# Kernel tuning notes

Measured on AMD Instinct MI355X. Metric: run time of the kernel, lower is better.

The kernel has to match this reference:

```python
import math
import jax, jax.numpy as jnp
import numpy as np

B = 1024
D = 384
Q = 65536
TOPK = 128
HARD_W = 2.0
TEMP_START = 0.2
TEMP_END = 0.05
WARMUP = 10


def _temperature(epoch):
    # curriculum cosine decay (epoch is a Python int)
    if epoch >= WARMUP:
        return TEMP_END
    progress = epoch / max(1, WARMUP)
    return TEMP_END + 0.5 * (TEMP_START - TEMP_END) * (1.0 + math.cos(math.pi * progress))


def _normalize(x):
    # F.normalize: x / max(||x||, eps)
    n = jnp.linalg.norm(x, axis=-1, keepdims=True)
    return x / jnp.maximum(n, 1e-12)


def _hard_neg_reweight(logits):
    # logits: [B, N]; labels = arange(B) (diagonal positives)
    b = logits.shape[0]
    rows = jnp.arange(b)
    neg_logits = logits.at[rows, rows].set(-jnp.inf)      # mask positives
    _, hard_idx = jax.lax.top_k(neg_logits, TOPK)          # [B, TOPK] hardest negatives
    weights = jnp.ones_like(logits)
    weights = weights.at[rows[:, None], hard_idx].set(HARD_W)
    weights = weights.at[rows, rows].set(1.0)
    return logits * weights


def _cross_entropy_diag(logits):
    b = logits.shape[0]
    logp = jax.nn.log_softmax(logits, axis=-1)
    return -jnp.mean(logp[jnp.arange(b), jnp.arange(b)])


def setup_inputs() -> dict:
    key = jax.random.key(0)
    k1, k2, k3, k4 = jax.random.split(key, 4)
    rgb_feat = jax.random.normal(k1, (B, D), dtype=jnp.float32)
    ir_feat = jax.random.normal(k2, (B, D), dtype=jnp.float32)
    rgb_queue = _normalize(jax.random.normal(k3, (Q, D), dtype=jnp.float32))
    ir_queue = _normalize(jax.random.normal(k4, (Q, D), dtype=jnp.float32))
    return {"rgb_feat": rgb_feat, "ir_feat": ir_feat,
            "rgb_queue": rgb_queue, "ir_queue": ir_queue, "epoch": 0}


def reference(rgb_feat, ir_feat, rgb_queue, ir_queue, epoch):
    temp = _temperature(epoch)
    rgb_z = _normalize(rgb_feat.astype(jnp.float32))
    ir_z = _normalize(ir_feat.astype(jnp.float32))
    ir_all = jnp.concatenate([ir_z, ir_queue], axis=0)    # [B+Q, D]
    rgb_all = jnp.concatenate([rgb_z, rgb_queue], axis=0)
    logits_r2i = (rgb_z @ ir_all.T) / temp                # [B, B+Q]
    logits_i2r = (ir_z @ rgb_all.T) / temp
    logits_r2i = _hard_neg_reweight(logits_r2i)
    logits_i2r = _hard_neg_reweight(logits_i2r)
    return 0.5 * (_cross_entropy_diag(logits_r2i) + _cross_entropy_diag(logits_i2r))
```

## Files before the change

### kernel.cpp

```cpp
#include <hip/hip_runtime.h>
#include <hip/hip_bf16.h>

#define B_    1024
#define D_    384
#define Q_    65536
#define N_    66560
#define TOPK_ 128

#define NBIN_ 4096
#define CAP_  2048

typedef __bf16 bf16x8 __attribute__((ext_vector_type(8)));
typedef float  f32x4  __attribute__((ext_vector_type(4)));
typedef unsigned short u16;
typedef u16 u16x8 __attribute__((ext_vector_type(8)));

__device__ __forceinline__ unsigned short f2bf(float x) {
  unsigned int u = __float_as_uint(x);
  unsigned int r = (u + 0x7fffu + ((u >> 16) & 1u)) >> 16;
  return (unsigned short)r;
}

__device__ __forceinline__ void gld_lds16(const void* g, void* l) {
  __builtin_amdgcn_global_load_lds(
      (__attribute__((address_space(1))) void*)(g),
      (__attribute__((address_space(3))) void*)(l), 16, 0, 0);
}

__device__ __forceinline__ void wait_vmcnt(int n) {
  switch (n) {
    case 12: asm volatile("s_waitcnt vmcnt(12)" ::: "memory"); break;
    case 6:  asm volatile("s_waitcnt vmcnt(6)"  ::: "memory"); break;
    default: asm volatile("s_waitcnt vmcnt(0)"  ::: "memory"); break;
  }
}

__device__ __forceinline__ unsigned int bf2key(unsigned int u) {
  return u ^ ((u & 0x8000u) ? 0xFFFFu : 0x8000u);
}

__global__ __launch_bounds__(64) void k_normalize(
    const float* __restrict__ rgb, const float* __restrict__ ir,
    const int* __restrict__ ep,
    u16* __restrict__ zrA, u16* __restrict__ ziA,
    u16* __restrict__ zrU, u16* __restrict__ ziU)
{
  int r = blockIdx.x & (B_ - 1);
  bool isIr = blockIdx.x >= B_;
  const float* src = (isIr ? ir : rgb) + (size_t)r * D_;
  u16* dA = (isIr ? ziA : zrA) + (size_t)r * D_;
  u16* dU = (isIr ? ziU : zrU) + (size_t)r * D_;
  int t = threadIdx.x;
  float x[6]; float ss = 0.f;
  #pragma unroll
  for (int k = 0; k < 6; ++k) { x[k] = src[t + 64*k]; ss += x[k]*x[k]; }
  #pragma unroll
  for (int off = 32; off > 0; off >>= 1) ss += __shfl_down(ss, off);
  ss = __shfl(ss, 0);
  float inv = 1.0f / fmaxf(sqrtf(ss), 1e-12f);

  int e = ep[0];
  float temp;
  if (e >= 10) temp = 0.05f;
  else {
    float p = (float)e * 0.1f;
    temp = 0.05f + 0.075f * (1.0f + cosf(3.14159265358979323846f * p));
  }
  float itemp = 1.0f / temp;

  #pragma unroll
  for (int k = 0; k < 6; ++k) {
    float z = x[k] * inv;
    dU[t + 64*k] = f2bf(z);
    dA[t + 64*k] = f2bf(z * itemp);
  }
}

__global__ __launch_bounds__(256) void k_build_ball(
    const u16* __restrict__ zU, const float* __restrict__ queue,
    u16* __restrict__ ball)
{
  size_t i = ((size_t)blockIdx.x * 256 + threadIdx.x) * 8;
  const size_t zElems = (size_t)B_ * D_;
  if (i < zElems) {
    *(uint4*)(ball + i) = *(const uint4*)(zU + i);
  } else {
    const float* q = queue + (i - zElems);
    float4 a = *(const float4*)q;
    float4 b = *(const float4*)(q + 4);
    u16x8 o;
    o[0] = f2bf(a.x); o[1] = f2bf(a.y); o[2] = f2bf(a.z); o[3] = f2bf(a.w);
    o[4] = f2bf(b.x); o[5] = f2bf(b.y); o[6] = f2bf(b.z); o[7] = f2bf(b.w);
    *(u16x8*)(ball + i) = o;
  }
}

#define BK_ 32
#define NSTEP_ 12
__global__ __launch_bounds__(256, 2) void k_gemm(
    const u16* __restrict__ A,
    const u16* __restrict__ ball,
    u16* __restrict__ C,
    float* __restrict__ diag,
    int r0, int mtiles)
{
  __shared__ __align__(16) unsigned char smem[73728];
  u16* Ct = (u16*)smem;

  int bid = blockIdx.x, nwg = gridDim.x;
  int xcd = bid & 7, loc = bid >> 3;
  int q = nwg >> 3, rr8 = nwg & 7;
  int wgid = (xcd < rr8 ? xcd * (q + 1) : rr8 * (q + 1) + (xcd - rr8) * q) + loc;
  int nt = wgid / mtiles;
  int mt = wgid - nt * mtiles;

  const int tid  = threadIdx.x;
  const int wave = tid >> 6, lane = tid & 63;
  const int mbase = mt * 128;
  const int nbase = nt * 256;
  const u16* Ab = A    + (size_t)(r0 + mbase) * D_;
  const u16* Bb = ball + (size_t)nbase * D_;

  auto As = [&](int t) -> u16* { return (u16*)(smem + (t % 3) * 24576); };
  auto Bs = [&](int t) -> u16* { return (u16*)(smem + (t % 3) * 24576 + 8192); };
  auto stage = [&](int t) {
    const int ks = t * BK_;
    #pragma unroll
    for (int i = 0; i < 2; ++i) {
      int f = i * 256 + tid;
      int rr = f >> 2, cc = f & 3;
      int koff = (((cc * 16) ^ (((rr >> 1) & 3) << 4)) >> 1);
      gld_lds16(Ab + (size_t)rr * D_ + ks + koff, As(t) + (size_t)f * 8);
    }
    #pragma unroll
    for (int i = 0; i < 4; ++i) {
      int f = i * 256 + tid;
      int rr = f >> 2, cc = f & 3;
      int koff = (((cc * 16) ^ (((rr >> 1) & 3) << 4)) >> 1);
      gld_lds16(Bb + (size_t)rr * D_ + ks + koff, Bs(t) + (size_t)f * 8);
    }
  };

  f32x4 acc[8][4];
  #pragma unroll
  for (int m = 0; m < 8; ++m)
    #pragma unroll
    for (int n = 0; n < 4; ++n)
      #pragma unroll
      for (int r = 0; r < 4; ++r) acc[m][n][r] = 0.0f;

  const int lr = lane & 15;
  const int kb = (lane >> 4) * 16;

  stage(0); stage(1);

  #pragma unroll
  for (int t = 0; t < NSTEP_; ++t) {
    if (t + 2 < NSTEP_) stage(t + 2);
    wait_vmcnt(t < NSTEP_ - 2 ? 12 : (t == NSTEP_ - 2 ? 6 : 0));
    __builtin_amdgcn_s_barrier();
    __builtin_amdgcn_sched_barrier(0);

    const u16* Ac = As(t);
    const u16* Bc = Bs(t);
    bf16x8 af[8], bq[4];
    #pragma unroll
    for (int m = 0; m < 8; ++m) {
      int row = m*16 + lr;
      af[m] = *(const bf16x8*)((const char*)Ac + row * 64 + (kb ^ (((row >> 1) & 3) << 4)));
    }
    #pragma unroll
    for (int n = 0; n < 4; ++n) {
      int row = wave*64 + n*16 + lr;
      bq[n] = *(const bf16x8*)((const char*)Bc + row * 64 + (kb ^ (((row >> 1) & 3) << 4)));
    }
    #pragma unroll
    for (int m = 0; m < 8; ++m)
      #pragma unroll
      for (int n = 0; n < 4; ++n)
        acc[m][n] = __builtin_amdgcn_mfma_f32_16x16x32_bf16(af[m], bq[n], acc[m][n], 0, 0, 0);

    asm volatile("s_waitcnt lgkmcnt(0)" ::: "memory");
    __builtin_amdgcn_sched_barrier(0);
    __builtin_amdgcn_s_barrier();
  }

  const int rowq = (lane >> 4) * 4;
  #pragma unroll
  for (int m = 0; m < 8; ++m) {
    #pragma unroll
    for (int n = 0; n < 4; ++n) {
      int lcol = wave*64 + n*16 + lr;
      int gcol = nbase + lcol;
      #pragma unroll
      for (int r = 0; r < 4; ++r) {
        int lrow = m*16 + rowq + r;
        float x = acc[m][n][r];
        int grow = r0 + mbase + lrow;
        if (gcol == grow) { diag[grow] = x; x = -60.0f; }
        Ct[lrow * 264 + lcol] = f2bf(x);
      }
    }
  }
  __syncthreads();

  #pragma unroll
  for (int j = 0; j < 16; ++j) {
    int id = j * 256 + tid;
    int row = id >> 5, cc8 = (id & 31) * 8;
    u16x8 v = *(const u16x8*)(Ct + row * 264 + cc8);
    *(u16x8*)(C + (size_t)(mbase + row) * N_ + nbase + cc8) = v;
  }
}

__global__ __launch_bounds__(256) void k_select(
    const u16* __restrict__ C, const float* __restrict__ diag,
    float* __restrict__ rowloss, int r0)
{
  __shared__ unsigned int hist[NBIN_];
  __shared__ float vals[CAP_];
  __shared__ float fred[256];
  __shared__ unsigned int csum[256];
  __shared__ int sh_bstar, sh_above, sh_cnt;

  const int t = threadIdx.x;
  const int grow = r0 + blockIdx.x;
  const u16x8* p = (const u16x8*)(C + (size_t)blockIdx.x * N_);

  uint4* h4 = (uint4*)hist;
  #pragma unroll
  for (int i = 0; i < 4; ++i) h4[i * 256 + t] = make_uint4(0,0,0,0);
  if (t == 0) sh_cnt = 0;
  __syncthreads();

  float es0 = 0.f, es1 = 0.f;
  #pragma unroll 1
  for (int base = 0; base < 8192; base += 2048) {
    u16x8 v[8];
    #pragma unroll
    for (int j = 0; j < 8; ++j) v[j] = p[base + j * 256 + t];
    #pragma unroll
    for (int j = 0; j < 8; ++j) {
      #pragma unroll
      for (int e = 0; e < 8; ++e) {
        unsigned int u = (unsigned int)(unsigned short)v[j][e];
        atomicAdd(&hist[bf2key(u) >> 4], 1u);
        float ex = __expf(__uint_as_float(u << 16));
        if (j & 1) es1 += ex; else es0 += ex;
      }
    }
  }
  if (t < 128) {
    u16x8 v = p[8192 + t];
    #pragma unroll
    for (int e = 0; e < 8; ++e) {
      unsigned int u = (unsigned int)(unsigned short)v[e];
      atomicAdd(&hist[bf2key(u) >> 4], 1u);
      es0 += __expf(__uint_as_float(u << 16));
    }
  }
  float esum = es0 + es1;
  __syncthreads();

  unsigned int S = 0;
  #pragma unroll
  for (int i = 0; i < 16; ++i) S += hist[t * 16 + i];
  csum[t] = S;
  __syncthreads();

  unsigned int a = S;
  #pragma unroll
  for (int s = 1; s < 256; s <<= 1) {
    unsigned int add = (t + s < 256) ? csum[t + s] : 0u;
    __syncthreads();
    a += add; csum[t] = a;
    __syncthreads();
  }

  int above_chunk = (t < 255) ? (int)csum[t + 1] : 0;
  if (above_chunk < TOPK_ && above_chunk + (int)S >= TOPK_) {
    int cum = above_chunk;
    #pragma unroll 1
    for (int i = 15; i >= 0; --i) {
      int c = (int)hist[t * 16 + i];
      if (cum + c >= TOPK_) { sh_bstar = t * 16 + i; sh_above = cum; break; }
      cum += c;
    }
  }
  __syncthreads();
  const unsigned int bstar = (unsigned int)sh_bstar;
  const int A = sh_above;

  float delta = 0.f;
  #pragma unroll 1
  for (int base = 0; base < 8192; base += 2048) {
    u16x8 v[8];
    #pragma unroll
    for (int j = 0; j < 8; ++j) v[j] = p[base + j * 256 + t];
    #pragma unroll
    for (int j = 0; j < 8; ++j) {
      #pragma unroll
      for (int e = 0; e < 8; ++e) {
        unsigned int u = (unsigned int)(unsigned short)v[j][e];
        unsigned int bin = bf2key(u) >> 4;
        if (bin >= bstar) {
          float val = __uint_as_float(u << 16);
          if (bin > bstar) delta += __expf(2.f * val) - __expf(val);
          else { int s = atomicAdd(&sh_cnt, 1); if (s < CAP_) vals[s] = val; }
        }
      }
    }
  }
  if (t < 128) {
    u16x8 v = p[8192 + t];
    #pragma unroll
    for (int e = 0; e < 8; ++e) {
      unsigned int u = (unsigned int)(unsigned short)v[e];
      unsigned int bin = bf2key(u) >> 4;
      if (bin >= bstar) {
        float val = __uint_as_float(u << 16);
        if (bin > bstar) delta += __expf(2.f * val) - __expf(val);
        else { int s = atomicAdd(&sh_cnt, 1); if (s < CAP_) vals[s] = val; }
      }
    }
  }
  __syncthreads();

  int C2 = sh_cnt < CAP_ ? sh_cnt : CAP_;
  int need = TOPK_ - A;
  for (int i = t; i < C2; i += 256) {
    float v = vals[i];
    int g = 0;
    for (int k = 0; k < C2; ++k)
      g += (vals[k] > v) || (vals[k] == v && k < i);
    if (g < need) delta += __expf(2.f * v) - __expf(v);
  }

  fred[t] = esum + delta;
  __syncthreads();
  #pragma unroll
  for (int s = 128; s > 0; s >>= 1) { if (t < s) fred[t] += fred[t + s]; __syncthreads(); }

  if (t == 0) {
    float d = diag[grow];
    rowloss[grow] = logf(fred[0] + __expf(d)) - d;
  }
}

__global__ __launch_bounds__(256) void k_final(
    const float* __restrict__ rowloss, float* __restrict__ out)
{
  __shared__ float red[256];
  int t = threadIdx.x;
  float s = 0.f;
  for (int i = t; i < 2 * B_; i += 256) s += rowloss[i];
  red[t] = s;
  __syncthreads();
  for (int k = 128; k > 0; k >>= 1) { if (t < k) red[t] += red[t + k]; __syncthreads(); }
  if (t == 0) out[0] = red[0] * (1.0f / (2.0f * B_));
}

extern "C" void kernel_launch(void* const* d_in, const int* in_sizes, int n_in,
                              void* d_out, int out_size, void* d_ws, size_t ws_size,
                              hipStream_t stream)
{
  const float* rgb_feat = (const float*)d_in[0];
  const float* ir_feat  = (const float*)d_in[1];
  const float* rgb_q    = (const float*)d_in[2];
  const float* ir_q     = (const float*)d_in[3];
  const int*   epoch    = (const int*)d_in[4];

  char* ws = (char*)d_ws;
  size_t off = 0;
  auto alloc = [&](size_t bytes) -> char* {
    char* p = ws + off;
    off = (off + bytes + 255) & ~(size_t)255;
    return p;
  };

  u16* zrA = (u16*)alloc((size_t)B_ * D_ * 2);
  u16* ziA = (u16*)alloc((size_t)B_ * D_ * 2);
  u16* zrU = (u16*)alloc((size_t)B_ * D_ * 2);
  u16* ziU = (u16*)alloc((size_t)B_ * D_ * 2);
  float* diag    = (float*)alloc((size_t)2 * B_ * 4);
  float* rowloss = (float*)alloc((size_t)2 * B_ * 4);
  u16* ball = (u16*)alloc((size_t)N_ * D_ * 2);

  size_t avail = ws_size > off ? ws_size - off : 0;
  int SR = (int)(avail / ((size_t)N_ * 2));
  SR &= ~127;
  if (SR > B_) SR = B_;
  if (SR < 128) SR = 128;
  u16* slab = (u16*)(ws + off);

  k_normalize<<<dim3(2 * B_), dim3(64), 0, stream>>>(
      rgb_feat, ir_feat, epoch, zrA, ziA, zrU, ziU);

  for (int dir = 0; dir < 2; ++dir) {
    const u16*   Amat   = (dir == 0) ? zrA : ziA;
    const u16*   zOther = (dir == 0) ? ziU : zrU;
    const float* queue  = (dir == 0) ? ir_q : rgb_q;
    float* diagD = diag    + dir * B_;
    float* lossD = rowloss + dir * B_;

    k_build_ball<<<dim3((unsigned)((size_t)N_ * D_ / 8 / 256)), dim3(256), 0, stream>>>(
        zOther, queue, ball);

    for (int r0 = 0; r0 < B_; r0 += SR) {
      int cur = (B_ - r0) < SR ? (B_ - r0) : SR;
      int mtiles = cur / 128;
      int nwg = (N_ / 256) * mtiles;
      k_gemm<<<dim3(nwg), dim3(256), 0, stream>>>(
          Amat, ball, slab, diagD, r0, mtiles);
      k_select<<<dim3(cur), dim3(256), 0, stream>>>(slab, diagD, lossD, r0);
    }
  }

  k_final<<<dim3(1), dim3(256), 0, stream>>>(rowloss, (float*)d_out);
}
```

Before: 318.5 us.

## Fuse GEMM, select and ball-build into one kernel to overlap stages

Merges the GEMM, top-k select and ball-building kernels into a single block-dispatched kernel. The schedule splits each direction into two 512-row halves with double slabs, so the select of one half runs in the same launch as the GEMM of the next half, and building the next direction's ball overlaps the last select. The GEMM now uses a two-stage LDS pipeline instead of three and writes its epilogue in two passes, cutting LDS to 48KB so three blocks fit per CU. The shallower prefetch may expose more load latency, and mixed block types can imbalance the CUs.

```diff
diff --git a/kernel.cpp b/kernel.cpp
--- a/kernel.cpp
+++ b/kernel.cpp
@@ -28,11 +28,8 @@
 }
 
 __device__ __forceinline__ void wait_vmcnt(int n) {
-  switch (n) {
-    case 12: asm volatile("s_waitcnt vmcnt(12)" ::: "memory"); break;
-    case 6:  asm volatile("s_waitcnt vmcnt(6)"  ::: "memory"); break;
-    default: asm volatile("s_waitcnt vmcnt(0)"  ::: "memory"); break;
-  }
+  if (n == 6) asm volatile("s_waitcnt vmcnt(6)" ::: "memory");
+  else        asm volatile("s_waitcnt vmcnt(0)" ::: "memory");
 }
 
 __device__ __forceinline__ unsigned int bf2key(unsigned int u) {
@@ -76,11 +73,261 @@
   }
 }
 
-__global__ __launch_bounds__(256) void k_build_ball(
-    const u16* __restrict__ zU, const float* __restrict__ queue,
+__device__ __forceinline__ void gemm_body(
+    unsigned char* smem, int bid,
+    const u16* __restrict__ A, const u16* __restrict__ ball,
+    u16* __restrict__ C, float* __restrict__ diag,
+    int r0, int mtiles, int nwg)
+{
+  int xcd = bid & 7, loc = bid >> 3;
+  int q = nwg >> 3, r8 = nwg & 7;
+  int wgid = (xcd < r8 ? xcd * (q + 1) : r8 * (q + 1) + (xcd - r8) * q) + loc;
+  int nt = wgid / mtiles;
+  int mt = wgid - nt * mtiles;
+
+  const int tid  = threadIdx.x;
+  const int wave = tid >> 6, lane = tid & 63;
+  const int mbase = mt * 128;
+  const int nbase = nt * 256;
+  const u16* Ab = A    + (size_t)(r0 + mbase) * D_;
+  const u16* Bb = ball + (size_t)nbase * D_;
+
+  u16* Ct = (u16*)smem;
+
+  auto As = [&](int t) -> u16* { return (u16*)(smem + (t & 1) * 24576); };
+  auto Bs = [&](int t) -> u16* { return (u16*)(smem + (t & 1) * 24576 + 8192); };
+  auto stage = [&](int t) {
+    const int ks = t * 32;
+    #pragma unroll
+    for (int i = 0; i < 2; ++i) {
+      int f = i * 256 + tid, rr = f >> 2, cc = f & 3;
+      int koff = (((cc * 16) ^ (((rr >> 1) & 3) << 4)) >> 1);
+      gld_lds16(Ab + (size_t)rr * D_ + ks + koff, As(t) + (size_t)f * 8);
+    }
+    #pragma unroll
+    for (int i = 0; i < 4; ++i) {
+      int f = i * 256 + tid, rr = f >> 2, cc = f & 3;
+      int koff = (((cc * 16) ^ (((rr >> 1) & 3) << 4)) >> 1);
+      gld_lds16(Bb + (size_t)rr * D_ + ks + koff, Bs(t) + (size_t)f * 8);
+    }
+  };
+
+  f32x4 acc[8][4];
+  #pragma unroll
+  for (int m = 0; m < 8; ++m)
+    #pragma unroll
+    for (int n = 0; n < 4; ++n)
+      #pragma unroll
+      for (int r = 0; r < 4; ++r) acc[m][n][r] = 0.0f;
+
+  const int lr = lane & 15;
+  const int kb = (lane >> 4) * 16;
+
+  stage(0); stage(1);
+
+  #pragma unroll
+  for (int t = 0; t < 12; ++t) {
+    wait_vmcnt(t < 11 ? 6 : 0);
+    __builtin_amdgcn_s_barrier();
+    __builtin_amdgcn_sched_barrier(0);
+
+    const u16* Ac = As(t);
+    const u16* Bc = Bs(t);
+    bf16x8 af[8], bq[4];
+    #pragma unroll
+    for (int m = 0; m < 8; ++m) {
+      int row = m*16 + lr;
+      af[m] = *(const bf16x8*)((const char*)Ac + row * 64 + (kb ^ (((row >> 1) & 3) << 4)));
+    }
+    #pragma unroll
+    for (int n = 0; n < 4; ++n) {
+      int row = wave*64 + n*16 + lr;
+      bq[n] = *(const bf16x8*)((const char*)Bc + row * 64 + (kb ^ (((row >> 1) & 3) << 4)));
+    }
+    #pragma unroll
+    for (int m = 0; m < 8; ++m)
+      #pragma unroll
+      for (int n = 0; n < 4; ++n)
+        acc[m][n] = __builtin_amdgcn_mfma_f32_16x16x32_bf16(af[m], bq[n], acc[m][n], 0, 0, 0);
+
+    asm volatile("s_waitcnt lgkmcnt(0)" ::: "memory");
+    __builtin_amdgcn_sched_barrier(0);
+    __builtin_amdgcn_s_barrier();
+    if (t + 2 < 12) stage(t + 2);
+  }
+
+  const int rowq = (lane >> 4) * 4;
+  #pragma unroll
+  for (int pass = 0; pass < 2; ++pass) {
+    if (pass) __syncthreads();
+    #pragma unroll
+    for (int mm = 0; mm < 4; ++mm) {
+      int m = pass * 4 + mm;
+      #pragma unroll
+      for (int n = 0; n < 4; ++n) {
+        int lcol = wave*64 + n*16 + lr;
+        int gcol = nbase + lcol;
+        #pragma unroll
+        for (int r = 0; r < 4; ++r) {
+          int lrow = m*16 + rowq + r;
+          float x = acc[m][n][r];
+          int grow = r0 + mbase + lrow;
+          if (gcol == grow) { diag[grow] = x; x = -60.0f; }
+          Ct[(lrow - pass*64) * 264 + lcol] = f2bf(x);
+        }
+      }
+    }
+    __syncthreads();
+    #pragma unroll
+    for (int j = 0; j < 8; ++j) {
+      int id = j * 256 + tid;
+      int row = id >> 5, cc8 = (id & 31) * 8;
+      u16x8 v = *(const u16x8*)(Ct + row * 264 + cc8);
+      *(u16x8*)(C + (size_t)(mbase + pass*64 + row) * N_ + nbase + cc8) = v;
+    }
+  }
+}
+
+__device__ __forceinline__ void select_body(
+    unsigned char* smem, int sbid,
+    const u16* __restrict__ C, const float* __restrict__ diag,
+    float* __restrict__ rowloss, int r0)
+{
+  unsigned int* hist = (unsigned int*)smem;
+  float*        vals = (float*)(smem + 16384);
+  float*        fred = (float*)(smem + 24576);
+  unsigned int* csum = (unsigned int*)(smem + 25600);
+  int*          shv  = (int*)(smem + 26624);
+
+  const int t = threadIdx.x;
+  const int grow = r0 + sbid;
+  const u16x8* p = (const u16x8*)(C + (size_t)sbid * N_);
+
+  uint4* h4 = (uint4*)hist;
+  #pragma unroll
+  for (int i = 0; i < 4; ++i) h4[i * 256 + t] = make_uint4(0,0,0,0);
+  if (t == 0) shv[2] = 0;
+  __syncthreads();
+
+  float es0 = 0.f, es1 = 0.f;
+  #pragma unroll 1
+  for (int base = 0; base < 8192; base += 2048) {
+    u16x8 v[8];
+    #pragma unroll
+    for (int j = 0; j < 8; ++j) v[j] = p[base + j * 256 + t];
+    #pragma unroll
+    for (int j = 0; j < 8; ++j) {
+      #pragma unroll
+      for (int e = 0; e < 8; ++e) {
+        unsigned int u = (unsigned int)(unsigned short)v[j][e];
+        atomicAdd(&hist[bf2key(u) >> 4], 1u);
+        float ex = __expf(__uint_as_float(u << 16));
+        if (j & 1) es1 += ex; else es0 += ex;
+      }
+    }
+  }
+  if (t < 128) {
+    u16x8 v = p[8192 + t];
+    #pragma unroll
+    for (int e = 0; e < 8; ++e) {
+      unsigned int u = (unsigned int)(unsigned short)v[e];
+      atomicAdd(&hist[bf2key(u) >> 4], 1u);
+      es0 += __expf(__uint_as_float(u << 16));
+    }
+  }
+  float esum = es0 + es1;
+  __syncthreads();
+
+  unsigned int S = 0;
+  #pragma unroll
+  for (int i = 0; i < 16; ++i) S += hist[t * 16 + i];
+  csum[t] = S;
+  __syncthreads();
+
+  unsigned int a = S;
+  #pragma unroll
+  for (int s = 1; s < 256; s <<= 1) {
+    unsigned int add = (t + s < 256) ? csum[t + s] : 0u;
+    __syncthreads();
+    a += add; csum[t] = a;
+    __syncthreads();
+  }
+
+  int above_chunk = (t < 255) ? (int)csum[t + 1] : 0;
+  if (above_chunk < TOPK_ && above_chunk + (int)S >= TOPK_) {
+    int cum = above_chunk;
+    #pragma unroll 1
+    for (int i = 15; i >= 0; --i) {
+      int c = (int)hist[t * 16 + i];
+      if (cum + c >= TOPK_) { shv[0] = t * 16 + i; shv[1] = cum; break; }
+      cum += c;
+    }
+  }
+  __syncthreads();
+  const unsigned int bstar = (unsigned int)shv[0];
+  const int A = shv[1];
+
+  float delta = 0.f;
+  #pragma unroll 1
+  for (int base = 0; base < 8192; base += 2048) {
+    u16x8 v[8];
+    #pragma unroll
+    for (int j = 0; j < 8; ++j) v[j] = p[base + j * 256 + t];
+    #pragma unroll
+    for (int j = 0; j < 8; ++j) {
+      #pragma unroll
+      for (int e = 0; e < 8; ++e) {
+        unsigned int u = (unsigned int)(unsigned short)v[j][e];
+        unsigned int bin = bf2key(u) >> 4;
+        if (bin >= bstar) {
+          float val = __uint_as_float(u << 16);
+          if (bin > bstar) delta += __expf(2.f * val) - __expf(val);
+          else { int s = atomicAdd(&shv[2], 1); if (s < CAP_) vals[s] = val; }
+        }
+      }
+    }
+  }
+  if (t < 128) {
+    u16x8 v = p[8192 + t];
+    #pragma unroll
+    for (int e = 0; e < 8; ++e) {
+      unsigned int u = (unsigned int)(unsigned short)v[e];
+      unsigned int bin = bf2key(u) >> 4;
+      if (bin >= bstar) {
+        float val = __uint_as_float(u << 16);
+        if (bin > bstar) delta += __expf(2.f * val) - __expf(val);
+        else { int s = atomicAdd(&shv[2], 1); if (s < CAP_) vals[s] = val; }
+      }
+    }
+  }
+  __syncthreads();
+
+  int C2 = shv[2] < CAP_ ? shv[2] : CAP_;
+  int need = TOPK_ - A;
+  for (int i = t; i < C2; i += 256) {
+    float v = vals[i];
+    int g = 0;
+    for (int k = 0; k < C2; ++k)
+      g += (vals[k] > v) || (vals[k] == v && k < i);
+    if (g < need) delta += __expf(2.f * v) - __expf(v);
+  }
+
+  fred[t] = esum + delta;
+  __syncthreads();
+  #pragma unroll
+  for (int s = 128; s > 0; s >>= 1) { if (t < s) fred[t] += fred[t + s]; __syncthreads(); }
+
+  if (t == 0) {
+    float d = diag[grow];
+    rowloss[grow] = logf(fred[0] + __expf(d)) - d;
+  }
+}
+
+__device__ __forceinline__ void ball_body(
+    int bbid, const u16* __restrict__ zU, const float* __restrict__ queue,
     u16* __restrict__ ball)
 {
-  size_t i = ((size_t)blockIdx.x * 256 + threadIdx.x) * 8;
+  size_t i = ((size_t)bbid * 256 + threadIdx.x) * 8;
   const size_t zElems = (size_t)B_ * D_;
   if (i < zElems) {
     *(uint4*)(ball + i) = *(const uint4*)(zU + i);
@@ -95,256 +342,25 @@
   }
 }
 
-#define BK_ 32
-#define NSTEP_ 12
-__global__ __launch_bounds__(256, 2) void k_gemm(
-    const u16* __restrict__ A,
-    const u16* __restrict__ ball,
-    u16* __restrict__ C,
-    float* __restrict__ diag,
-    int r0, int mtiles)
-{
-  __shared__ __align__(16) unsigned char smem[73728];
-  u16* Ct = (u16*)smem;
-
-  int bid = blockIdx.x, nwg = gridDim.x;
-  int xcd = bid & 7, loc = bid >> 3;
-  int q = nwg >> 3, rr8 = nwg & 7;
-  int wgid = (xcd < rr8 ? xcd * (q + 1) : rr8 * (q + 1) + (xcd - rr8) * q) + loc;
-  int nt = wgid / mtiles;
-  int mt = wgid - nt * mtiles;
-
-  const int tid  = threadIdx.x;
-  const int wave = tid >> 6, lane = tid & 63;
-  const int mbase = mt * 128;
-  const int nbase = nt * 256;
-  const u16* Ab = A    + (size_t)(r0 + mbase) * D_;
-  const u16* Bb = ball + (size_t)nbase * D_;
-
-  auto As = [&](int t) -> u16* { return (u16*)(smem + (t % 3) * 24576); };
-  auto Bs = [&](int t) -> u16* { return (u16*)(smem + (t % 3) * 24576 + 8192); };
-  auto stage = [&](int t) {
-    const int ks = t * BK_;
-    #pragma unroll
-    for (int i = 0; i < 2; ++i) {
-      int f = i * 256 + tid;
-      int rr = f >> 2, cc = f & 3;
-      int koff = (((cc * 16) ^ (((rr >> 1) & 3) << 4)) >> 1);
-      gld_lds16(Ab + (size_t)rr * D_ + ks + koff, As(t) + (size_t)f * 8);
-    }
-    #pragma unroll
-    for (int i = 0; i < 4; ++i) {
-      int f = i * 256 + tid;
-      int rr = f >> 2, cc = f & 3;
-      int koff = (((cc * 16) ^ (((rr >> 1) & 3) << 4)) >> 1);
-      gld_lds16(Bb + (size_t)rr * D_ + ks + koff, Bs(t) + (size_t)f * 8);
-    }
-  };
-
-  f32x4 acc[8][4];
-  #pragma unroll
-  for (int m = 0; m < 8; ++m)
-    #pragma unroll
-    for (int n = 0; n < 4; ++n)
-      #pragma unroll
-      for (int r = 0; r < 4; ++r) acc[m][n][r] = 0.0f;
-
-  const int lr = lane & 15;
-  const int kb = (lane >> 4) * 16;
-
-  stage(0); stage(1);
-
-  #pragma unroll
-  for (int t = 0; t < NSTEP_; ++t) {
-    if (t + 2 < NSTEP_) stage(t + 2);
-    wait_vmcnt(t < NSTEP_ - 2 ? 12 : (t == NSTEP_ - 2 ? 6 : 0));
-    __builtin_amdgcn_s_barrier();
-    __builtin_amdgcn_sched_barrier(0);
-
-    const u16* Ac = As(t);
-    const u16* Bc = Bs(t);
-    bf16x8 af[8], bq[4];
-    #pragma unroll
-    for (int m = 0; m < 8; ++m) {
-      int row = m*16 + lr;
-      af[m] = *(const bf16x8*)((const char*)Ac + row * 64 + (kb ^ (((row >> 1) & 3) << 4)));
-    }
-    #pragma unroll
-    for (int n = 0; n < 4; ++n) {
-      int row = wave*64 + n*16 + lr;
-      bq[n] = *(const bf16x8*)((const char*)Bc + row * 64 + (kb ^ (((row >> 1) & 3) << 4)));
-    }
-    #pragma unroll
-    for (int m = 0; m < 8; ++m)
-      #pragma unroll
-      for (int n = 0; n < 4; ++n)
-        acc[m][n] = __builtin_amdgcn_mfma_f32_16x16x32_bf16(af[m], bq[n], acc[m][n], 0, 0, 0);
-
-    asm volatile("s_waitcnt lgkmcnt(0)" ::: "memory");
-    __builtin_amdgcn_sched_barrier(0);
-    __builtin_amdgcn_s_barrier();
-  }
-
-  const int rowq = (lane >> 4) * 4;
-  #pragma unroll
-  for (int m = 0; m < 8; ++m) {
-    #pragma unroll
-    for (int n = 0; n < 4; ++n) {
-      int lcol = wave*64 + n*16 + lr;
-      int gcol = nbase + lcol;
-      #pragma unroll
-      for (int r = 0; r < 4; ++r) {
-        int lrow = m*16 + rowq + r;
-        float x = acc[m][n][r];
-        int grow = r0 + mbase + lrow;
-        if (gcol == grow) { diag[grow] = x; x = -60.0f; }
-        Ct[lrow * 264 + lcol] = f2bf(x);
-      }
-    }
-  }
-  __syncthreads();
-
-  #pragma unroll
-  for (int j = 0; j < 16; ++j) {
-    int id = j * 256 + tid;
-    int row = id >> 5, cc8 = (id & 31) * 8;
-    u16x8 v = *(const u16x8*)(Ct + row * 264 + cc8);
-    *(u16x8*)(C + (size_t)(mbase + row) * N_ + nbase + cc8) = v;
-  }
-}
-
-__global__ __launch_bounds__(256) void k_select(
-    const u16* __restrict__ C, const float* __restrict__ diag,
-    float* __restrict__ rowloss, int r0)
-{
-  __shared__ unsigned int hist[NBIN_];
-  __shared__ float vals[CAP_];
-  __shared__ float fred[256];
-  __shared__ unsigned int csum[256];
-  __shared__ int sh_bstar, sh_above, sh_cnt;
-
-  const int t = threadIdx.x;
-  const int grow = r0 + blockIdx.x;
-  const u16x8* p = (const u16x8*)(C + (size_t)blockIdx.x * N_);
-
-  uint4* h4 = (uint4*)hist;
-  #pragma unroll
-  for (int i = 0; i < 4; ++i) h4[i * 256 + t] = make_uint4(0,0,0,0);
-  if (t == 0) sh_cnt = 0;
-  __syncthreads();
-
-  float es0 = 0.f, es1 = 0.f;
-  #pragma unroll 1
-  for (int base = 0; base < 8192; base += 2048) {
-    u16x8 v[8];
-    #pragma unroll
-    for (int j = 0; j < 8; ++j) v[j] = p[base + j * 256 + t];
-    #pragma unroll
-    for (int j = 0; j < 8; ++j) {
-      #pragma unroll
-      for (int e = 0; e < 8; ++e) {
-        unsigned int u = (unsigned int)(unsigned short)v[j][e];
-        atomicAdd(&hist[bf2key(u) >> 4], 1u);
-        float ex = __expf(__uint_as_float(u << 16));
-        if (j & 1) es1 += ex; else es0 += ex;
-      }
-    }
-  }
-  if (t < 128) {
-    u16x8 v = p[8192 + t];
-    #pragma unroll
-    for (int e = 0; e < 8; ++e) {
-      unsigned int u = (unsigned int)(unsigned short)v[e];
-      atomicAdd(&hist[bf2key(u) >> 4], 1u);
-      es0 += __expf(__uint_as_float(u << 16));
-    }
-  }
-  float esum = es0 + es1;
-  __syncthreads();
-
-  unsigned int S = 0;
-  #pragma unroll
-  for (int i = 0; i < 16; ++i) S += hist[t * 16 + i];
-  csum[t] = S;
-  __syncthreads();
-
-  unsigned int a = S;
-  #pragma unroll
-  for (int s = 1; s < 256; s <<= 1) {
-    unsigned int add = (t + s < 256) ? csum[t + s] : 0u;
-    __syncthreads();
-    a += add; csum[t] = a;
-    __syncthreads();
-  }
-
-  int above_chunk = (t < 255) ? (int)csum[t + 1] : 0;
-  if (above_chunk < TOPK_ && above_chunk + (int)S >= TOPK_) {
-    int cum = above_chunk;
-    #pragma unroll 1
-    for (int i = 15; i >= 0; --i) {
-      int c = (int)hist[t * 16 + i];
-      if (cum + c >= TOPK_) { sh_bstar = t * 16 + i; sh_above = cum; break; }
-      cum += c;
-    }
-  }
-  __syncthreads();
-  const unsigned int bstar = (unsigned int)sh_bstar;
-  const int A = sh_above;
-
-  float delta = 0.f;
-  #pragma unroll 1
-  for (int base = 0; base < 8192; base += 2048) {
-    u16x8 v[8];
-    #pragma unroll
-    for (int j = 0; j < 8; ++j) v[j] = p[base + j * 256 + t];
-    #pragma unroll
-    for (int j = 0; j < 8; ++j) {
-      #pragma unroll
-      for (int e = 0; e < 8; ++e) {
-        unsigned int u = (unsigned int)(unsigned short)v[j][e];
-        unsigned int bin = bf2key(u) >> 4;
-        if (bin >= bstar) {
-          float val = __uint_as_float(u << 16);
-          if (bin > bstar) delta += __expf(2.f * val) - __expf(val);
-          else { int s = atomicAdd(&sh_cnt, 1); if (s < CAP_) vals[s] = val; }
-        }
-      }
-    }
-  }
-  if (t < 128) {
-    u16x8 v = p[8192 + t];
-    #pragma unroll
-    for (int e = 0; e < 8; ++e) {
-      unsigned int u = (unsigned int)(unsigned short)v[e];
-      unsigned int bin = bf2key(u) >> 4;
-      if (bin >= bstar) {
-        float val = __uint_as_float(u << 16);
-        if (bin > bstar) delta += __expf(2.f * val) - __expf(val);
-        else { int s = atomicAdd(&sh_cnt, 1); if (s < CAP_) vals[s] = val; }
-      }
-    }
-  }
-  __syncthreads();
-
-  int C2 = sh_cnt < CAP_ ? sh_cnt : CAP_;
-  int need = TOPK_ - A;
-  for (int i = t; i < C2; i += 256) {
-    float v = vals[i];
-    int g = 0;
-    for (int k = 0; k < C2; ++k)
-      g += (vals[k] > v) || (vals[k] == v && k < i);
-    if (g < need) delta += __expf(2.f * v) - __expf(v);
-  }
-
-  fred[t] = esum + delta;
-  __syncthreads();
-  #pragma unroll
-  for (int s = 128; s > 0; s >>= 1) { if (t < s) fred[t] += fred[t + s]; __syncthreads(); }
-
-  if (t == 0) {
-    float d = diag[grow];
-    rowloss[grow] = logf(fred[0] + __expf(d)) - d;
-  }
+__global__ __launch_bounds__(256, 3) void k_fused(
+    const u16* gA, const u16* gBall, u16* gC, float* gDiag,
+    int g_r0, int g_mtiles, int g_nwg,
+    const u16* sC, const float* sDiag, float* sRow, int s_r0, int s_nblk,
+    const u16* bZ, const float* bQ, u16* bBall, int b_nblk)
+{
+  __shared__ __align__(16) unsigned char smem[49152];
+  int bid = blockIdx.x;
+  if (bid < g_nwg) {
+    gemm_body(smem, bid, gA, gBall, gC, gDiag, g_r0, g_mtiles, g_nwg);
+    return;
+  }
+  bid -= g_nwg;
+  if (bid < s_nblk) {
+    select_body(smem, bid, sC, sDiag, sRow, s_r0);
+    return;
+  }
+  bid -= s_nblk;
+  if (bid < b_nblk) ball_body(bid, bZ, bQ, bBall);
 }
 
 __global__ __launch_bounds__(256) void k_final(
@@ -387,32 +403,79 @@
   u16* ball = (u16*)alloc((size_t)N_ * D_ * 2);
 
   size_t avail = ws_size > off ? ws_size - off : 0;
-  int SR = (int)(avail / ((size_t)N_ * 2));
-  SR &= ~127;
-  if (SR > B_) SR = B_;
-  if (SR < 128) SR = 128;
-  u16* slab = (u16*)(ws + off);
+  const size_t halfBytes = (size_t)512 * N_ * 2;
+  const int NBALL = (int)(((size_t)N_ * D_ / 8) / 256);
+  const u16* Z16 = nullptr; const float* F32 = nullptr;
 
   k_normalize<<<dim3(2 * B_), dim3(64), 0, stream>>>(
       rgb_feat, ir_feat, epoch, zrA, ziA, zrU, ziU);
 
-  for (int dir = 0; dir < 2; ++dir) {
-    const u16*   Amat   = (dir == 0) ? zrA : ziA;
-    const u16*   zOther = (dir == 0) ? ziU : zrU;
-    const float* queue  = (dir == 0) ? ir_q : rgb_q;
-    float* diagD = diag    + dir * B_;
-    float* lossD = rowloss + dir * B_;
-
-    k_build_ball<<<dim3((unsigned)((size_t)N_ * D_ / 8 / 256)), dim3(256), 0, stream>>>(
-        zOther, queue, ball);
-
-    for (int r0 = 0; r0 < B_; r0 += SR) {
-      int cur = (B_ - r0) < SR ? (B_ - r0) : SR;
-      int mtiles = cur / 128;
-      int nwg = (N_ / 256) * mtiles;
-      k_gemm<<<dim3(nwg), dim3(256), 0, stream>>>(
-          Amat, ball, slab, diagD, r0, mtiles);
-      k_select<<<dim3(cur), dim3(256), 0, stream>>>(slab, diagD, lossD, r0);
+  if (avail >= 2 * halfBytes) {
+    u16* slabA = (u16*)(ws + off);
+    u16* slabB = slabA + (size_t)512 * N_;
+    float* dg0 = diag;        float* dg1 = diag + B_;
+    float* ls0 = rowloss;     float* ls1 = rowloss + B_;
+
+    k_fused<<<dim3(NBALL), dim3(256), 0, stream>>>(
+        Z16, Z16, nullptr, nullptr, 0, 1, 0,
+        Z16, F32, nullptr, 0, 0,
+        ziU, ir_q, ball, NBALL);
+    k_fused<<<dim3(1040), dim3(256), 0, stream>>>(
+        zrA, ball, slabA, dg0, 0, 4, 1040,
+        Z16, F32, nullptr, 0, 0,
+        Z16, F32, nullptr, 0);
+    k_fused<<<dim3(1040 + 512), dim3(256), 0, stream>>>(
+        zrA, ball, slabB, dg0, 512, 4, 1040,
+        slabA, dg0, ls0, 0, 512,
+        Z16, F32, nullptr, 0);
+    k_fused<<<dim3(512 + NBALL), dim3(256), 0, stream>>>(
+        Z16, Z16, nullptr, nullptr, 0, 1, 0,
+        slabB, dg0, ls0, 512, 512,
+        zrU, rgb_q, ball, NBALL);
+    k_fused<<<dim3(1040), dim3(256), 0, stream>>>(
+        ziA, ball, slabA, dg1, 0, 4, 1040,
+        Z16, F32, nullptr, 0, 0,
+        Z16, F32, nullptr, 0);
+    k_fused<<<dim3(1040 + 512), dim3(256), 0, stream>>>(
+        ziA, ball, slabB, dg1, 512, 4, 1040,
+        slabA, dg1, ls1, 0, 512,
+        Z16, F32, nullptr, 0);
+    k_fused<<<dim3(512), dim3(256), 0, stream>>>(
+        Z16, Z16, nullptr, nullptr, 0, 1, 0,
+        slabB, dg1, ls1, 512, 512,
+        Z16, F32, nullptr, 0);
+  } else {
+    int SR = (int)(avail / ((size_t)N_ * 2));
+    SR &= ~127;
+    if (SR > B_) SR = B_;
+    if (SR < 128) SR = 128;
+    u16* slab = (u16*)(ws + off);
+
+    for (int dir = 0; dir < 2; ++dir) {
+      const u16*   Amat   = (dir == 0) ? zrA : ziA;
+      const u16*   zOther = (dir == 0) ? ziU : zrU;
+      const float* queue  = (dir == 0) ? ir_q : rgb_q;
+      float* dg = diag    + dir * B_;
+      float* ls = rowloss + dir * B_;
+
+      k_fused<<<dim3(NBALL), dim3(256), 0, stream>>>(
+          Z16, Z16, nullptr, nullptr, 0, 1, 0,
+          Z16, F32, nullptr, 0, 0,
+          zOther, queue, ball, NBALL);
+
+      for (int r0 = 0; r0 < B_; r0 += SR) {
+        int cur = (B_ - r0) < SR ? (B_ - r0) : SR;
+        int mtiles = cur / 128;
+        int nwg = (N_ / 256) * mtiles;
+        k_fused<<<dim3(nwg), dim3(256), 0, stream>>>(
+            Amat, ball, slab, dg, r0, mtiles, nwg,
+            Z16, F32, nullptr, 0, 0,
+            Z16, F32, nullptr, 0);
+        k_fused<<<dim3(cur), dim3(256), 0, stream>>>(
+            Z16, Z16, nullptr, nullptr, 0, 1, 0,
+            slab, dg, ls, r0, cur,
+            Z16, F32, nullptr, 0);
+      }
     }
   }
 
```

New measurement: 466.5 us. +46.5%, slower.
